# Optimization experiments

Hardware: AMD Instinct MI355X
Metric: run time of the kernel (lower is better)

Reference implementation:

```python
import jax, jax.numpy as jnp
import numpy as np

EMBED_DIM = 384
NUM_HEADS = 6
HEAD_DIM = EMBED_DIM // NUM_HEADS
SCALE = HEAD_DIM ** (-0.5)


def setup_inputs() -> dict:
    key = jax.random.key(0)
    ks = jax.random.split(key, 5)
    B, N, D = 8, 2048, EMBED_DIM
    x = jax.random.normal(ks[0], (B, N, D), dtype=jnp.float32)
    # Linear params, torch convention: weight [out, in], bias [out]
    w_qkv = jax.random.normal(ks[1], (3 * D, D), dtype=jnp.float32) * (D ** -0.5)
    b_qkv = jax.random.normal(ks[2], (3 * D,), dtype=jnp.float32) * 0.01
    w_out = jax.random.normal(ks[3], (D, D), dtype=jnp.float32) * (D ** -0.5)
    b_out = jax.random.normal(ks[4], (D,), dtype=jnp.float32) * 0.01
    return {"x": x, "w_qkv": w_qkv, "b_qkv": b_qkv, "w_out": w_out, "b_out": b_out}


def reference(x, w_qkv, b_qkv, w_out, b_out):
    B, N, D = x.shape
    H, Dh = NUM_HEADS, HEAD_DIM
    # qkv projection: [B,N,3D]
    qkv = jnp.einsum('bnd,ed->bne', x, w_qkv) + b_qkv
    qkv = qkv.reshape(B, N, 3, H, Dh).transpose(2, 0, 3, 1, 4)  # [3,B,H,N,Dh]
    q, k, v = qkv[0], qkv[1], qkv[2]
    # full NxN attention scores (faithful to original eager math)
    scores = jnp.einsum('bhnd,bhmd->bhnm', q, k) * SCALE  # [B,H,N,N]
    attn = jax.nn.softmax(scores, axis=-1)
    out = jnp.einsum('bhnm,bhmd->bhnd', attn, v)  # [B,H,N,Dh]
    out = out.transpose(0, 2, 1, 3).reshape(B, N, D)
    out = jnp.einsum('bnd,ed->bne', out, w_out) + b_out
    return out
```

## Files before the change

kernel.cpp:

```cpp
#include <hip/hip_runtime.h>

typedef unsigned short u16;
typedef unsigned int u32;
typedef float f32x4 __attribute__((ext_vector_type(4)));
typedef __bf16 bf16x8 __attribute__((ext_vector_type(8)));
typedef unsigned short u16x8 __attribute__((ext_vector_type(8)));
typedef unsigned short u16x4 __attribute__((ext_vector_type(4)));
typedef unsigned int u32x4 __attribute__((ext_vector_type(4)));

__device__ inline u16 f2bf(float f) {
    return __builtin_bit_cast(u16, (__bf16)f);
}

__device__ inline void gll16(const u16* g, u16* l) {
    u16* gnc = const_cast<u16*>(g);
    __builtin_amdgcn_global_load_lds((__attribute__((address_space(1))) u32*)gnc,
                                     (__attribute__((address_space(3))) u32*)l,
                                     16, 0, 0);
}

#define MFMA(a, b, c) __builtin_amdgcn_mfma_f32_16x16x32_bf16((a), (b), (c), 0, 0, 0)

#define C_SHIFT 17.3123405f
#define Q_SCALE 0.1803368801f

__global__ __launch_bounds__(256)
void cvt_kernel(const float* __restrict__ X, const float* __restrict__ Wq,
                const float* __restrict__ Wo, u16* __restrict__ Xb,
                u16* __restrict__ Wqb, u16* __restrict__ Wob)
{
    int i = blockIdx.x * 256 + threadIdx.x;
    const float* src; u16* dst; int off;
    if (i < 1572864)       { src = X;  dst = Xb;  off = i; }
    else if (i < 1683456)  { src = Wq; dst = Wqb; off = i - 1572864; }
    else                   { src = Wo; dst = Wob; off = i - 1683456; }
    f32x4 v = *(const f32x4*)&src[off * 4];
    u16x4 p;
    for (int k = 0; k < 4; ++k) p[k] = f2bf(v[k]);
    *(u16x4*)&dst[off * 4] = p;
}

__global__ __launch_bounds__(256)
void qkv_kernel(const u16* __restrict__ Xb, const u16* __restrict__ Wqb,
                const float* __restrict__ B, u16* __restrict__ Qo,
                u16* __restrict__ Ko, u16* __restrict__ VTo)
{
    __shared__ __align__(128) u16 As[128][64];
    __shared__ __align__(128) u16 Ws[128][64];
    const int tid = threadIdx.x;
    const int m0 = blockIdx.x * 128;
    const int n0 = blockIdx.y * 128;
    const int wv = tid >> 6, lane = tid & 63;
    const int l15 = lane & 15, quad = lane >> 4;
    const int mw = (wv & 1) * 64, nw = (wv >> 1) * 64;

    const int lr = lane >> 3;
    const int gsrc = (lane & 7) ^ lr;
    const int swz = (quad ^ (l15 & 7)) * 8;

    f32x4 acc[4][4] = {};
    for (int kt = 0; kt < 384; kt += 64) {
        __syncthreads();
#pragma unroll
        for (int i = 0; i < 4; ++i) {
            int r = (wv * 4 + i) * 8 + lr;
            gll16(&Xb[(m0 + r) * 384 + kt + gsrc * 8], &As[(wv * 4 + i) * 8][0]);
            gll16(&Wqb[(n0 + r) * 384 + kt + gsrc * 8], &Ws[(wv * 4 + i) * 8][0]);
        }
        __syncthreads();
#pragma unroll
        for (int kc = 0; kc < 2; ++kc) {
            bf16x8 a[4], bf[4];
#pragma unroll
            for (int mi = 0; mi < 4; ++mi)
                a[mi] = *(const bf16x8*)&As[mw + mi * 16 + l15][swz ^ (kc << 5)];
#pragma unroll
            for (int nj = 0; nj < 4; ++nj)
                bf[nj] = *(const bf16x8*)&Ws[nw + nj * 16 + l15][swz ^ (kc << 5)];
#pragma unroll
            for (int mi = 0; mi < 4; ++mi)
#pragma unroll
                for (int nj = 0; nj < 4; ++nj)
                    acc[mi][nj] = MFMA(a[mi], bf[nj], acc[mi][nj]);
        }
    }
    for (int nj = 0; nj < 4; ++nj) {
        int col = n0 + nw + nj * 16 + l15;
        int t = col / 384;
        int h = (col % 384) / 64, dh = col & 63;
        float bias = B[col];
        for (int mi = 0; mi < 4; ++mi)
            for (int r = 0; r < 4; ++r) {
                int gm = m0 + mw + mi * 16 + quad * 4 + r;
                int bb = gm >> 11, n = gm & 2047;
                int bh = bb * 6 + h;
                float v = acc[mi][nj][r] + bias;
                if (t == 0)      Qo[(bh * 2048 + n) * 64 + dh] = f2bf(v * Q_SCALE);
                else if (t == 1) Ko[(bh * 2048 + n) * 64 + dh] = f2bf(v);
                else {
                    int nn = (n & ~31) | (((n >> 2) & 3) << 3)
                           | (((n >> 4) & 1) << 2) | (n & 3);
                    VTo[(bh * 64 + dh) * 2048 + nn] = f2bf(v);
                }
            }
    }
}

__global__ __launch_bounds__(512)
void attn_kernel(const u16* __restrict__ Q, const u16* __restrict__ K,
                 const u16* __restrict__ VT, u16* __restrict__ O)
{
    __shared__ __align__(128) u16 Ks[2][64][64];
    __shared__ __align__(128) u16 VTs[2][64][64];
    __shared__ __align__(16) float lbuf[128];

    const int tid = threadIdx.x;
    const int lin = blockIdx.y * 16 + blockIdx.x;
    const int lin2 = (lin & 7) * 96 + (lin >> 3);
    const int bh = lin2 >> 4;
    const int q0 = (lin2 & 15) * 128;
    const int wv = tid >> 6, lane = tid & 63;
    const int l15 = lane & 15, quad = lane >> 4;
    const int qsub = wv & 3, kh = wv >> 2;

    bf16x8 qf[2][2];
#pragma unroll
    for (int qb = 0; qb < 2; ++qb) {
        const u16* qptr = &Q[(bh * 2048 + q0 + qsub * 32 + qb * 16 + l15) * 64 + quad * 8];
        qf[qb][0] = *(const bf16x8*)qptr;
        qf[qb][1] = *(const bf16x8*)(qptr + 32);
    }

    const int lr = lane >> 3;
    const int gsrc = (lane & 7) ^ lr;
    const u16* ksrc = &K[(bh * 2048 + wv * 8 + lr) * 64 + gsrc * 8];
    const u16* vsrc = &VT[(bh * 64 + wv * 8 + lr) * 2048 + gsrc * 8];
    const int swz = (quad ^ (l15 & 7)) * 8;

    const f32x4 cinit = {-C_SHIFT, -C_SHIFT, -C_SHIFT, -C_SHIFT};
    float l_part[2] = {};
    f32x4 acc[2][4] = {};

    gll16(ksrc, &Ks[0][wv * 8][0]);
    gll16(vsrc, &VTs[0][wv * 8][0]);

    for (int j = 0; j < 32; ++j) {
        const int cur = j & 1;
        __syncthreads();
        if (j < 31) {
            gll16(ksrc + (j + 1) * 4096, &Ks[cur ^ 1][wv * 8][0]);
            gll16(vsrc + (j + 1) * 64, &VTs[cur ^ 1][wv * 8][0]);
        }

        u32 w[2][2][2];
#pragma unroll
        for (int c = 0; c < 2; ++c) {
            const u16* krow = &Ks[cur][kh * 32 + c * 16 + l15][0];
            bf16x8 a0 = *(const bf16x8*)(krow + swz);
            bf16x8 a1 = *(const bf16x8*)(krow + (swz ^ 32));
#pragma unroll
            for (int qb = 0; qb < 2; ++qb) {
                f32x4 s = MFMA(a0, qf[qb][0], cinit);
                s = MFMA(a1, qf[qb][1], s);
                float p0 = __builtin_amdgcn_exp2f(s[0]);
                float p1 = __builtin_amdgcn_exp2f(s[1]);
                float p2 = __builtin_amdgcn_exp2f(s[2]);
                float p3 = __builtin_amdgcn_exp2f(s[3]);
                l_part[qb] += p0;
                l_part[qb] += p1;
                l_part[qb] += p2;
                l_part[qb] += p3;
                w[qb][c][0] = (u32)f2bf(p0) | ((u32)f2bf(p1) << 16);
                w[qb][c][1] = (u32)f2bf(p2) | ((u32)f2bf(p3) << 16);
            }
        }

        bf16x8 pf[2];
#pragma unroll
        for (int qb = 0; qb < 2; ++qb) {
            u32x4 t = {w[qb][0][0], w[qb][0][1], w[qb][1][0], w[qb][1][1]};
            pf[qb] = __builtin_bit_cast(bf16x8, t);
        }

#pragma unroll
        for (int ct = 0; ct < 4; ++ct) {
            bf16x8 bv = *(const bf16x8*)(&VTs[cur][ct * 16 + l15][0] + (swz ^ (kh << 5)));
#pragma unroll
            for (int qb = 0; qb < 2; ++qb)
                acc[qb][ct] = MFMA(pf[qb], bv, acc[qb][ct]);
        }
    }

    float lh[2];
#pragma unroll
    for (int qb = 0; qb < 2; ++qb) {
        float t = l_part[qb];
        t += __shfl_xor(t, 16);
        t += __shfl_xor(t, 32);
        lh[qb] = t;
    }
    __syncthreads();
    if (kh == 1) {
        float* sb = (qsub < 2) ? (float*)&Ks[qsub][0][0] : (float*)&VTs[qsub - 2][0][0];
#pragma unroll
        for (int qb = 0; qb < 2; ++qb)
#pragma unroll
            for (int ct = 0; ct < 4; ++ct)
                *(f32x4*)&sb[((qb * 4 + ct) * 64 + lane) * 4] = acc[qb][ct];
        if (quad == 0) {
            lbuf[qsub * 32 + l15] = lh[0];
            lbuf[qsub * 32 + 16 + l15] = lh[1];
        }
    }
    __syncthreads();
    if (kh == 0) {
        float* sb = (qsub < 2) ? (float*)&Ks[qsub][0][0] : (float*)&VTs[qsub - 2][0][0];
#pragma unroll
        for (int qb = 0; qb < 2; ++qb)
#pragma unroll
            for (int ct = 0; ct < 4; ++ct)
                acc[qb][ct] += *(const f32x4*)&sb[((qb * 4 + ct) * 64 + lane) * 4];
        lh[0] += lbuf[qsub * 32 + l15];
        lh[1] += lbuf[qsub * 32 + 16 + l15];
        int b = bh / 6, h = bh % 6;
#pragma unroll
        for (int qb = 0; qb < 2; ++qb) {
            float li[4];
            for (int r = 0; r < 4; ++r) li[r] = 1.0f / __shfl(lh[qb], quad * 4 + r);
            for (int ct = 0; ct < 4; ++ct)
                for (int r = 0; r < 4; ++r) {
                    int row = q0 + qsub * 32 + qb * 16 + quad * 4 + r;
                    int dh = ct * 16 + l15;
                    O[(b * 2048 + row) * 384 + h * 64 + dh] = f2bf(acc[qb][ct][r] * li[r]);
                }
        }
    }
}

__global__ __launch_bounds__(256)
void outproj_kernel(const u16* __restrict__ A, const u16* __restrict__ Wob,
                    const float* __restrict__ B, float* __restrict__ out)
{
    __shared__ __align__(16) u16 As[64][72];
    __shared__ __align__(16) u16 Ws[64][72];
    const int tid = threadIdx.x;
    const int m0 = blockIdx.x * 64;
    const int n0 = blockIdx.y * 64;
    const int wv = tid >> 6, lane = tid & 63;
    const int l15 = lane & 15, quad = lane >> 4;

    f32x4 acc[4] = {};
    for (int kt = 0; kt < 384; kt += 64) {
        __syncthreads();
        for (int c = tid; c < 512; c += 256) {
            int row = c >> 3, cc = (c & 7) * 8;
            *(u16x8*)&As[row][cc] = *(const u16x8*)&A[(m0 + row) * 384 + kt + cc];
            *(u16x8*)&Ws[row][cc] = *(const u16x8*)&Wob[(n0 + row) * 384 + kt + cc];
        }
        __syncthreads();
        for (int kc = 0; kc < 2; ++kc) {
            bf16x8 b = *(const bf16x8*)&Ws[wv * 16 + l15][kc * 32 + quad * 8];
            for (int mi = 0; mi < 4; ++mi) {
                bf16x8 a = *(const bf16x8*)&As[mi * 16 + l15][kc * 32 + quad * 8];
                acc[mi] = MFMA(a, b, acc[mi]);
            }
        }
    }
    const int col = n0 + wv * 16 + l15;
    const float bias = B[col];
    for (int mi = 0; mi < 4; ++mi)
        for (int r = 0; r < 4; ++r) {
            int gm = m0 + mi * 16 + quad * 4 + r;
            out[gm * 384 + col] = acc[mi][r] + bias;
        }
}

extern "C" void kernel_launch(void* const* d_in, const int* in_sizes, int n_in,
                              void* d_out, int out_size, void* d_ws, size_t ws_size,
                              hipStream_t stream) {
    const float* x     = (const float*)d_in[0];
    const float* w_qkv = (const float*)d_in[1];
    const float* b_qkv = (const float*)d_in[2];
    const float* w_out = (const float*)d_in[3];
    const float* b_out = (const float*)d_in[4];
    float* out = (float*)d_out;

    char* ws = (char*)d_ws;
    u16* Qw   = (u16*)(ws);
    u16* Kw   = (u16*)(ws + 12582912);
    u16* VTw  = (u16*)(ws + 25165824);
    u16* XbAw = (u16*)(ws + 37748736);
    u16* Wqb  = (u16*)(ws + 50331648);
    u16* Wob  = (u16*)(ws + 51216384);

    cvt_kernel<<<6720, 256, 0, stream>>>(x, w_qkv, w_out, XbAw, Wqb, Wob);
    qkv_kernel<<<dim3(128, 9), 256, 0, stream>>>(XbAw, Wqb, b_qkv, Qw, Kw, VTw);
    attn_kernel<<<dim3(16, 48), 512, 0, stream>>>(Qw, Kw, VTw, XbAw);
    outproj_kernel<<<dim3(256, 6), 256, 0, stream>>>(XbAw, Wob, b_out, out);
}
```

Before: 206.0 us.

## Double-buffer LDS in QKV and out-proj GEMMs, retile out-proj to 128x128

Result: slower. 220.4 us (+7.0%).

```diff
diff --git a/kernel.cpp b/kernel.cpp
--- a/kernel.cpp
+++ b/kernel.cpp
@@ -45,11 +45,13 @@
                 const float* __restrict__ B, u16* __restrict__ Qo,
                 u16* __restrict__ Ko, u16* __restrict__ VTo)
 {
-    __shared__ __align__(128) u16 As[128][64];
-    __shared__ __align__(128) u16 Ws[128][64];
+    __shared__ __align__(128) u16 As[2][128][64];
+    __shared__ __align__(128) u16 Ws[2][128][64];
     const int tid = threadIdx.x;
-    const int m0 = blockIdx.x * 128;
-    const int n0 = blockIdx.y * 128;
+    const int lin = blockIdx.y * 128 + blockIdx.x;
+    const int lin2 = (lin & 7) * 144 + (lin >> 3);
+    const int m0 = (lin2 & 127) * 128;
+    const int n0 = (lin2 >> 7) * 128;
     const int wv = tid >> 6, lane = tid & 63;
     const int l15 = lane & 15, quad = lane >> 4;
     const int mw = (wv & 1) * 64, nw = (wv >> 1) * 64;
@@ -58,25 +60,36 @@
     const int gsrc = (lane & 7) ^ lr;
     const int swz = (quad ^ (l15 & 7)) * 8;
 
+    const u16* xb = &Xb[(m0 + 0) * 384 + gsrc * 8];
+    const u16* wb = &Wqb[(n0 + 0) * 384 + gsrc * 8];
+
     f32x4 acc[4][4] = {};
-    for (int kt = 0; kt < 384; kt += 64) {
+#pragma unroll
+    for (int i = 0; i < 4; ++i) {
+        int r = (wv * 4 + i) * 8 + lr;
+        gll16(xb + r * 384, &As[0][(wv * 4 + i) * 8][0]);
+        gll16(wb + r * 384, &Ws[0][(wv * 4 + i) * 8][0]);
+    }
+    for (int t = 0; t < 6; ++t) {
+        const int cur = t & 1;
         __syncthreads();
-#pragma unroll
-        for (int i = 0; i < 4; ++i) {
-            int r = (wv * 4 + i) * 8 + lr;
-            gll16(&Xb[(m0 + r) * 384 + kt + gsrc * 8], &As[(wv * 4 + i) * 8][0]);
-            gll16(&Wqb[(n0 + r) * 384 + kt + gsrc * 8], &Ws[(wv * 4 + i) * 8][0]);
-        }
-        __syncthreads();
+        if (t < 5) {
+#pragma unroll
+            for (int i = 0; i < 4; ++i) {
+                int r = (wv * 4 + i) * 8 + lr;
+                gll16(xb + r * 384 + (t + 1) * 64, &As[cur ^ 1][(wv * 4 + i) * 8][0]);
+                gll16(wb + r * 384 + (t + 1) * 64, &Ws[cur ^ 1][(wv * 4 + i) * 8][0]);
+            }
+        }
 #pragma unroll
         for (int kc = 0; kc < 2; ++kc) {
             bf16x8 a[4], bf[4];
 #pragma unroll
             for (int mi = 0; mi < 4; ++mi)
-                a[mi] = *(const bf16x8*)&As[mw + mi * 16 + l15][swz ^ (kc << 5)];
+                a[mi] = *(const bf16x8*)&As[cur][mw + mi * 16 + l15][swz ^ (kc << 5)];
 #pragma unroll
             for (int nj = 0; nj < 4; ++nj)
-                bf[nj] = *(const bf16x8*)&Ws[nw + nj * 16 + l15][swz ^ (kc << 5)];
+                bf[nj] = *(const bf16x8*)&Ws[cur][nw + nj * 16 + l15][swz ^ (kc << 5)];
 #pragma unroll
             for (int mi = 0; mi < 4; ++mi)
 #pragma unroll
@@ -241,38 +254,67 @@
 void outproj_kernel(const u16* __restrict__ A, const u16* __restrict__ Wob,
                     const float* __restrict__ B, float* __restrict__ out)
 {
-    __shared__ __align__(16) u16 As[64][72];
-    __shared__ __align__(16) u16 Ws[64][72];
+    __shared__ __align__(128) u16 As[2][128][64];
+    __shared__ __align__(128) u16 Ws[2][128][64];
     const int tid = threadIdx.x;
-    const int m0 = blockIdx.x * 64;
-    const int n0 = blockIdx.y * 64;
+    const int lin = blockIdx.y * 128 + blockIdx.x;
+    const int lin2 = (lin & 7) * 48 + (lin >> 3);
+    const int m0 = (lin2 & 127) * 128;
+    const int n0 = (lin2 >> 7) * 128;
     const int wv = tid >> 6, lane = tid & 63;
     const int l15 = lane & 15, quad = lane >> 4;
-
-    f32x4 acc[4] = {};
-    for (int kt = 0; kt < 384; kt += 64) {
+    const int mw = (wv & 1) * 64, nw = (wv >> 1) * 64;
+
+    const int lr = lane >> 3;
+    const int gsrc = (lane & 7) ^ lr;
+    const int swz = (quad ^ (l15 & 7)) * 8;
+
+    const u16* ab = &A[m0 * 384 + gsrc * 8];
+    const u16* wb = &Wob[n0 * 384 + gsrc * 8];
+
+    f32x4 acc[4][4] = {};
+#pragma unroll
+    for (int i = 0; i < 4; ++i) {
+        int r = (wv * 4 + i) * 8 + lr;
+        gll16(ab + r * 384, &As[0][(wv * 4 + i) * 8][0]);
+        gll16(wb + r * 384, &Ws[0][(wv * 4 + i) * 8][0]);
+    }
+    for (int t = 0; t < 6; ++t) {
+        const int cur = t & 1;
         __syncthreads();
-        for (int c = tid; c < 512; c += 256) {
-            int row = c >> 3, cc = (c & 7) * 8;
-            *(u16x8*)&As[row][cc] = *(const u16x8*)&A[(m0 + row) * 384 + kt + cc];
-            *(u16x8*)&Ws[row][cc] = *(const u16x8*)&Wob[(n0 + row) * 384 + kt + cc];
-        }
-        __syncthreads();
+        if (t < 5) {
+#pragma unroll
+            for (int i = 0; i < 4; ++i) {
+                int r = (wv * 4 + i) * 8 + lr;
+                gll16(ab + r * 384 + (t + 1) * 64, &As[cur ^ 1][(wv * 4 + i) * 8][0]);
+                gll16(wb + r * 384 + (t + 1) * 64, &Ws[cur ^ 1][(wv * 4 + i) * 8][0]);
+            }
+        }
+#pragma unroll
         for (int kc = 0; kc < 2; ++kc) {
-            bf16x8 b = *(const bf16x8*)&Ws[wv * 16 + l15][kc * 32 + quad * 8];
-            for (int mi = 0; mi < 4; ++mi) {
-                bf16x8 a = *(const bf16x8*)&As[mi * 16 + l15][kc * 32 + quad * 8];
-                acc[mi] = MFMA(a, b, acc[mi]);
-            }
-        }
-    }
-    const int col = n0 + wv * 16 + l15;
-    const float bias = B[col];
-    for (int mi = 0; mi < 4; ++mi)
-        for (int r = 0; r < 4; ++r) {
-            int gm = m0 + mi * 16 + quad * 4 + r;
-            out[gm * 384 + col] = acc[mi][r] + bias;
-        }
+            bf16x8 a[4], bf[4];
+#pragma unroll
+            for (int mi = 0; mi < 4; ++mi)
+                a[mi] = *(const bf16x8*)&As[cur][mw + mi * 16 + l15][swz ^ (kc << 5)];
+#pragma unroll
+            for (int nj = 0; nj < 4; ++nj)
+                bf[nj] = *(const bf16x8*)&Ws[cur][nw + nj * 16 + l15][swz ^ (kc << 5)];
+#pragma unroll
+            for (int mi = 0; mi < 4; ++mi)
+#pragma unroll
+                for (int nj = 0; nj < 4; ++nj)
+                    acc[mi][nj] = MFMA(a[mi], bf[nj], acc[mi][nj]);
+        }
+    }
+    for (int nj = 0; nj < 4; ++nj) {
+        const int col = n0 + nw + nj * 16 + l15;
+        const float bias = B[col];
+        for (int mi = 0; mi < 4; ++mi)
+            for (int r = 0; r < 4; ++r) {
+                int gm = m0 + mw + mi * 16 + quad * 4 + r;
+                out[gm * 384 + col] = acc[mi][nj][r] + bias;
+            }
+    }
 }
 
 extern "C" void kernel_launch(void* const* d_in, const int* in_sizes, int n_in,
@@ -296,5 +338,5 @@
     cvt_kernel<<<6720, 256, 0, stream>>>(x, w_qkv, w_out, XbAw, Wqb, Wob);
     qkv_kernel<<<dim3(128, 9), 256, 0, stream>>>(XbAw, Wqb, b_qkv, Qw, Kw, VTw);
     attn_kernel<<<dim3(16, 48), 512, 0, stream>>>(Qw, Kw, VTw, XbAw);
-    outproj_kernel<<<dim3(256, 6), 256, 0, stream>>>(XbAw, Wob, b_out, out);
-}
+    outproj_kernel<<<dim3(128, 3), 256, 0, stream>>>(XbAw, Wob, b_out, out);
+}
```
